# Performance work log

Hardware: AMD Instinct MI355X
Metric: run time of the kernel (lower is better)

Reference implementation:

```python
import jax, jax.numpy as jnp
import numpy as np

TOTAL_SIZE = 8192
K = 10
D_MODEL = 256
BATCH = 32


def setup_inputs() -> dict:
    key = jax.random.key(0)
    k1, k2 = jax.random.split(key)
    x = jax.random.normal(k1, (BATCH, TOTAL_SIZE, D_MODEL), dtype=jnp.float32)
    embedding = jax.random.normal(k2, (K, D_MODEL), dtype=jnp.float32) * 0.1
    interval = TOTAL_SIZE / K
    mu = jnp.asarray(np.arange(K, dtype=np.float32) * interval).reshape(1, K)
    sigma = jnp.full((1, K), 50.0, dtype=jnp.float32)
    return {"x": x, "embedding": embedding, "mu": mu, "sigma": sigma}


def reference(x, embedding, mu, sigma):
    # positions: (total_size, 1) broadcast against (1, K)
    positions = jnp.arange(TOTAL_SIZE, dtype=jnp.float32)[:, None]
    a = positions - mu                                   # (T, K)
    log_p = -jnp.square(a) / (2.0 * sigma + 1e-08) - jnp.log(jnp.abs(sigma) + 1e-08) / 2.0
    M = jax.nn.softmax(log_p, axis=1)                    # (T, K)
    pos_enc = M @ embedding                              # (T, d_model)
    return x + pos_enc[None, :, :]
```

## Files before the change

### kernel.cpp

```cpp
#include <hip/hip_runtime.h>
#include <math.h>

#define T_TOTAL 8192
#define KK      10
#define DMODEL  256
#define BATCH   32
#define TPB     4
#define D4      (DMODEL/4)
#define BSTRIDE4 ((size_t)T_TOTAL * D4)
#define BG      8

typedef float f32x4 __attribute__((ext_vector_type(4)));

__global__ __launch_bounds__(256) void gre_pos_add(
    const float* __restrict__ x,
    const float* __restrict__ emb,
    const float* __restrict__ mu,
    const float* __restrict__ sigma,
    float* __restrict__ out)
{
    const int tid = threadIdx.x;
    const int tl  = tid >> 6;
    const int c   = tid & 63;
    const int t   = blockIdx.x * TPB + tl;
    const int b0  = blockIdx.y * BG;

    float lp[KK];
    float mx = -INFINITY;
#pragma unroll
    for (int k = 0; k < KK; ++k) {
        const float mk = mu[k];
        const float sk = sigma[k];
        const float a  = (float)t - mk;
        const float v  = -(a * a) / (2.0f * sk + 1e-8f)
                         - 0.5f * __logf(fabsf(sk) + 1e-8f);
        lp[k] = v;
        mx = fmaxf(mx, v);
    }
    float s = 0.0f;
#pragma unroll
    for (int k = 0; k < KK; ++k) {
        lp[k] = __expf(lp[k] - mx);
        s += lp[k];
    }
    const float inv = 1.0f / s;

    const f32x4* __restrict__ emb4 = (const f32x4*)emb;
    f32x4 pe = (f32x4){0.f, 0.f, 0.f, 0.f};
#pragma unroll
    for (int k = 0; k < KK; ++k) {
        const f32x4 e = emb4[k * D4 + c];
        const float w = lp[k] * inv;
        pe += w * e;
    }

    const f32x4* __restrict__ x4 = (const f32x4*)x;
    f32x4* __restrict__ o4       = (f32x4*)out;
    const size_t base = (size_t)t * D4 + c + (size_t)b0 * BSTRIDE4;

    f32x4 v[BG];
#pragma unroll
    for (int i = 0; i < BG; ++i) {
        v[i] = x4[base + (size_t)i * BSTRIDE4];
    }
#pragma unroll
    for (int i = 0; i < BG; ++i) {
        f32x4 r = v[i] + pe;
        __builtin_nontemporal_store(r, &o4[base + (size_t)i * BSTRIDE4]);
    }
}

extern "C" void kernel_launch(void* const* d_in, const int* in_sizes, int n_in,
                              void* d_out, int out_size, void* d_ws, size_t ws_size,
                              hipStream_t stream) {
    const float* x     = (const float*)d_in[0];
    const float* emb   = (const float*)d_in[1];
    const float* mu    = (const float*)d_in[2];
    const float* sigma = (const float*)d_in[3];
    float* out         = (float*)d_out;

    dim3 grid(T_TOTAL / TPB, BATCH / BG);
    gre_pos_add<<<grid, 256, 0, stream>>>(x, emb, mu, sigma, out);
}
```

Baseline: 88.84 us.

## Split into PE table build kernel plus flat streaming add kernel

Precomputes the positional-encoding table (8 MB) into workspace with a separate kernel, then runs a flat, fully contiguous streaming add that reads x and the table, using the fused kernel only when workspace is too small. The goal is to drop the per-block softmax recompute and get perfectly linear memory access in the bandwidth-bound add. In exchange it adds a second launch, writes and re-reads the table, and depends on workspace size.

```diff
diff --git a/kernel.cpp b/kernel.cpp
--- a/kernel.cpp
+++ b/kernel.cpp
@@ -5,25 +5,25 @@
 #define KK      10
 #define DMODEL  256
 #define BATCH   32
-#define TPB     4
 #define D4      (DMODEL/4)
-#define BSTRIDE4 ((size_t)T_TOTAL * D4)
-#define BG      8
+#define PE4     (T_TOTAL * D4)
+#define PE_BYTES ((size_t)PE4 * 16)
+#define TOT4    ((size_t)BATCH * PE4)
+#define J_PER_THREAD 8
+#define BLK4    (256 * J_PER_THREAD)
 
 typedef float f32x4 __attribute__((ext_vector_type(4)));
 
-__global__ __launch_bounds__(256) void gre_pos_add(
-    const float* __restrict__ x,
+__global__ __launch_bounds__(256) void gre_pe_build(
     const float* __restrict__ emb,
     const float* __restrict__ mu,
     const float* __restrict__ sigma,
-    float* __restrict__ out)
+    f32x4* __restrict__ pe4)
 {
     const int tid = threadIdx.x;
     const int tl  = tid >> 6;
     const int c   = tid & 63;
-    const int t   = blockIdx.x * TPB + tl;
-    const int b0  = blockIdx.y * BG;
+    const int t   = blockIdx.x * 4 + tl;
 
     float lp[KK];
     float mx = -INFINITY;
@@ -49,24 +49,77 @@
     f32x4 pe = (f32x4){0.f, 0.f, 0.f, 0.f};
 #pragma unroll
     for (int k = 0; k < KK; ++k) {
-        const f32x4 e = emb4[k * D4 + c];
-        const float w = lp[k] * inv;
-        pe += w * e;
+        pe += (lp[k] * inv) * emb4[k * D4 + c];
     }
+    pe4[t * D4 + c] = pe;
+}
+
+__global__ __launch_bounds__(256) void gre_stream_add(
+    const f32x4* __restrict__ x4,
+    const f32x4* __restrict__ pe4,
+    f32x4* __restrict__ o4)
+{
+    const size_t base = (size_t)blockIdx.x * BLK4 + threadIdx.x;
+
+    f32x4 v[J_PER_THREAD];
+#pragma unroll
+    for (int j = 0; j < J_PER_THREAD; ++j)
+        v[j] = x4[base + (size_t)j * 256];
+
+#pragma unroll
+    for (int j = 0; j < J_PER_THREAD; ++j) {
+        const size_t idx = base + (size_t)j * 256;
+        f32x4 r = v[j] + pe4[idx & (size_t)(PE4 - 1)];
+        __builtin_nontemporal_store(r, &o4[idx]);
+    }
+}
+
+__global__ __launch_bounds__(256) void gre_fused(
+    const float* __restrict__ x,
+    const float* __restrict__ emb,
+    const float* __restrict__ mu,
+    const float* __restrict__ sigma,
+    float* __restrict__ out)
+{
+    const int tid = threadIdx.x;
+    const int tl  = tid >> 6;
+    const int c   = tid & 63;
+    const int t   = blockIdx.x * 4 + tl;
+    const int b0  = blockIdx.y * 8;
+
+    float lp[KK];
+    float mx = -INFINITY;
+#pragma unroll
+    for (int k = 0; k < KK; ++k) {
+        const float mk = mu[k];
+        const float sk = sigma[k];
+        const float a  = (float)t - mk;
+        const float v  = -(a * a) / (2.0f * sk + 1e-8f)
+                         - 0.5f * __logf(fabsf(sk) + 1e-8f);
+        lp[k] = v;
+        mx = fmaxf(mx, v);
+    }
+    float s = 0.0f;
+#pragma unroll
+    for (int k = 0; k < KK; ++k) { lp[k] = __expf(lp[k] - mx); s += lp[k]; }
+    const float inv = 1.0f / s;
+
+    const f32x4* __restrict__ emb4 = (const f32x4*)emb;
+    f32x4 pe = (f32x4){0.f, 0.f, 0.f, 0.f};
+#pragma unroll
+    for (int k = 0; k < KK; ++k) pe += (lp[k] * inv) * emb4[k * D4 + c];
 
     const f32x4* __restrict__ x4 = (const f32x4*)x;
     f32x4* __restrict__ o4       = (f32x4*)out;
-    const size_t base = (size_t)t * D4 + c + (size_t)b0 * BSTRIDE4;
+    const size_t base = (size_t)t * D4 + c + (size_t)b0 * PE4;
 
-    f32x4 v[BG];
+    f32x4 v[8];
 #pragma unroll
-    for (int i = 0; i < BG; ++i) {
-        v[i] = x4[base + (size_t)i * BSTRIDE4];
-    }
+    for (int i = 0; i < 8; ++i) v[i] = x4[base + (size_t)i * PE4];
 #pragma unroll
-    for (int i = 0; i < BG; ++i) {
+    for (int i = 0; i < 8; ++i) {
         f32x4 r = v[i] + pe;
-        __builtin_nontemporal_store(r, &o4[base + (size_t)i * BSTRIDE4]);
+        __builtin_nontemporal_store(r, &o4[base + (size_t)i * PE4]);
     }
 }
 
@@ -79,6 +132,14 @@
     const float* sigma = (const float*)d_in[3];
     float* out         = (float*)d_out;
 
-    dim3 grid(T_TOTAL / TPB, BATCH / BG);
-    gre_pos_add<<<grid, 256, 0, stream>>>(x, emb, mu, sigma, out);
+    if (ws_size >= PE_BYTES) {
+        f32x4* pe4 = (f32x4*)d_ws;
+        gre_pe_build<<<T_TOTAL / 4, 256, 0, stream>>>(emb, mu, sigma, pe4);
+        const int blocks = (int)(TOT4 / BLK4);
+        gre_stream_add<<<blocks, 256, 0, stream>>>(
+            (const f32x4*)x, (const f32x4*)pe4, (f32x4*)out);
+    } else {
+        dim3 grid(T_TOTAL / 4, BATCH / 8);
+        gre_fused<<<grid, 256, 0, stream>>>(x, emb, mu, sigma, out);
+    }
 }
```

Measured after the change: 100.5 us. 1.13x slower.

## Stream contiguous chunks per block and share softmax weights via LDS

Applied to the files above, without the earlier changes.

Each block now handles a contiguous 32-row chunk of the flattened tensor instead of strided batch slices. The x loads are issued first so their latency overlaps the softmax, which is computed once per row and kept in shared memory. Each thread then rebuilds its positional encoding from the shared weights and embedding values held in registers. The aim is a purely sequential memory access pattern with more blocks and more bytes in flight, at the cost of recomputing the positional encoding per batch and adding a block barrier.

```diff
diff --git a/kernel.cpp b/kernel.cpp
--- a/kernel.cpp
+++ b/kernel.cpp
@@ -5,68 +5,73 @@
 #define KK      10
 #define DMODEL  256
 #define BATCH   32
-#define TPB     4
 #define D4      (DMODEL/4)
-#define BSTRIDE4 ((size_t)T_TOTAL * D4)
-#define BG      8
+#define PE4     (T_TOTAL * D4)
+#define TOT4    ((size_t)BATCH * PE4)
+#define JPT     8
+#define CHUNK4  (256 * JPT)
+#define ROWS_PB 32
 
 typedef float f32x4 __attribute__((ext_vector_type(4)));
 
-__global__ __launch_bounds__(256) void gre_pos_add(
-    const float* __restrict__ x,
+__global__ __launch_bounds__(256) void gre_stream_fused(
+    const f32x4* __restrict__ x4,
     const float* __restrict__ emb,
     const float* __restrict__ mu,
     const float* __restrict__ sigma,
-    float* __restrict__ out)
+    f32x4* __restrict__ o4)
 {
     const int tid = threadIdx.x;
-    const int tl  = tid >> 6;
-    const int c   = tid & 63;
-    const int t   = blockIdx.x * TPB + tl;
-    const int b0  = blockIdx.y * BG;
+    const size_t base = (size_t)blockIdx.x * CHUNK4 + tid;
 
-    float lp[KK];
-    float mx = -INFINITY;
+    f32x4 v[JPT];
 #pragma unroll
-    for (int k = 0; k < KK; ++k) {
-        const float mk = mu[k];
-        const float sk = sigma[k];
-        const float a  = (float)t - mk;
-        const float v  = -(a * a) / (2.0f * sk + 1e-8f)
-                         - 0.5f * __logf(fabsf(sk) + 1e-8f);
-        lp[k] = v;
-        mx = fmaxf(mx, v);
-    }
-    float s = 0.0f;
+    for (int j = 0; j < JPT; ++j)
+        v[j] = x4[base + (size_t)j * 256];
+
+    __shared__ float wsm[ROWS_PB][KK];
+    {
+        const int r = tid >> 3;
+        const int t = ((blockIdx.x * ROWS_PB) & (T_TOTAL - 1)) + r;
+        float lp[KK];
+        float mx = -INFINITY;
 #pragma unroll
-    for (int k = 0; k < KK; ++k) {
-        lp[k] = __expf(lp[k] - mx);
-        s += lp[k];
-    }
-    const float inv = 1.0f / s;
-
-    const f32x4* __restrict__ emb4 = (const f32x4*)emb;
-    f32x4 pe = (f32x4){0.f, 0.f, 0.f, 0.f};
+        for (int k = 0; k < KK; ++k) {
+            const float mk = mu[k];
+            const float sk = sigma[k];
+            const float a  = (float)t - mk;
+            const float val = -(a * a) / (2.0f * sk + 1e-8f)
+                              - 0.5f * __logf(fabsf(sk) + 1e-8f);
+            lp[k] = val;
+            mx = fmaxf(mx, val);
+        }
+        float s = 0.0f;
 #pragma unroll
-    for (int k = 0; k < KK; ++k) {
-        const f32x4 e = emb4[k * D4 + c];
-        const float w = lp[k] * inv;
-        pe += w * e;
+        for (int k = 0; k < KK; ++k) { lp[k] = __expf(lp[k] - mx); s += lp[k]; }
+        const float inv = 1.0f / s;
+        const int k0 = tid & 7;
+        wsm[r][k0] = lp[k0] * inv;
+        if (k0 < 2) wsm[r][8 + k0] = lp[8 + k0] * inv;
     }
 
-    const f32x4* __restrict__ x4 = (const f32x4*)x;
-    f32x4* __restrict__ o4       = (f32x4*)out;
-    const size_t base = (size_t)t * D4 + c + (size_t)b0 * BSTRIDE4;
+    const int c = tid & 63;
+    const f32x4* __restrict__ emb4 = (const f32x4*)emb;
+    f32x4 e[KK];
+#pragma unroll
+    for (int k = 0; k < KK; ++k)
+        e[k] = emb4[k * D4 + c];
 
-    f32x4 v[BG];
+    __syncthreads();
+
 #pragma unroll
-    for (int i = 0; i < BG; ++i) {
-        v[i] = x4[base + (size_t)i * BSTRIDE4];
-    }
+    for (int j = 0; j < JPT; ++j) {
+        const int r = (tid >> 6) + 4 * j;
+        f32x4 pe = (f32x4){0.f, 0.f, 0.f, 0.f};
 #pragma unroll
-    for (int i = 0; i < BG; ++i) {
-        f32x4 r = v[i] + pe;
-        __builtin_nontemporal_store(r, &o4[base + (size_t)i * BSTRIDE4]);
+        for (int k = 0; k < KK; ++k)
+            pe += wsm[r][k] * e[k];
+        f32x4 res = v[j] + pe;
+        __builtin_nontemporal_store(res, &o4[base + (size_t)j * 256]);
     }
 }
 
@@ -79,6 +84,7 @@
     const float* sigma = (const float*)d_in[3];
     float* out         = (float*)d_out;
 
-    dim3 grid(T_TOTAL / TPB, BATCH / BG);
-    gre_pos_add<<<grid, 256, 0, stream>>>(x, emb, mu, sigma, out);
+    const int blocks = (int)(TOT4 / CHUNK4);
+    gre_stream_fused<<<blocks, 256, 0, stream>>>(
+        (const f32x4*)x, emb, mu, sigma, (f32x4*)out);
 }
```

After: 81.76 us. 1.09x faster.
